# Kernel optimization log

Measured on AMD Instinct MI355X. Metric: run time of the kernel, lower is better.

## Reference

```python
import math
import jax, jax.numpy as jnp
import numpy as np

N_LAYER = 6
THETA = 2.0 ** 16
LN_EPS = 1e-5


def _ln(x):
    # LayerNorm over last dim, no affine (elementwise_affine=False)
    mu = x.mean(-1, keepdims=True)
    var = ((x - mu) ** 2).mean(-1, keepdims=True)
    return (x - mu) / jnp.sqrt(var + LN_EPS)


def _rope(phases, v):
    # phases: (T, N); v: (B, H, T, N)
    ph = (phases % 1.0) * (2.0 * math.pi)
    c, s = jnp.cos(ph), jnp.sin(ph)
    v2 = v.reshape(v.shape[:-1] + (-1, 2))
    v_rot = jnp.stack((-v2[..., 1], v2[..., 0]), axis=-1).reshape(v.shape)
    return v * c + v_rot * s


def setup_inputs() -> dict:
    key = jax.random.key(0)
    ks = jax.random.split(key, 6)
    B, T, D, nh, mult, V = 2, 512, 256, 4, 64, 256
    N = D * mult // nh  # 4096 neurons per head
    std = 0.02
    return {
        "input_ids": jax.random.randint(ks[0], (B, T), 0, V, dtype=jnp.int64),
        "embed_table": jax.random.normal(ks[1], (V, D), jnp.float32) * std,
        "encoder": jax.random.normal(ks[2], (nh, D, N), jnp.float32) * std,
        "encoder_v": jax.random.normal(ks[3], (nh, D, N), jnp.float32) * std,
        "decoder": jax.random.normal(ks[4], (nh * N, D), jnp.float32) * std,
        "lm_head": jax.random.normal(ks[5], (D, V), jnp.float32) * std,
    }


def reference(input_ids, embed_table, encoder, encoder_v, decoder, lm_head):
    B, T = input_ids.shape
    nh, D, N = encoder.shape
    # RoPE freqs: quantize(arange(N), 2) / N exponent (matches get_freqs)
    qidx = jnp.floor(jnp.arange(N, dtype=jnp.float32) / 2.0) * 2.0
    freqs = 1.0 / (THETA ** (qidx / N)) / (2.0 * math.pi)
    phases = jnp.arange(T, dtype=jnp.float32)[:, None] * freqs[None, :]  # (T, N)
    # strictly-lower causal mask (tril with diagonal=-1)
    causal = jnp.tril(jnp.ones((T, T), dtype=bool), k=-1)
    dec = decoder.reshape(nh, N, D)  # head-major, matches transpose(1,2).reshape

    x = _ln(embed_table[input_ids])[:, None]  # (B, 1, T, D)
    trace = None
    for _ in range(N_LAYER):  # shared (tied) weights across layers
        x_sparse = jax.nn.relu(jnp.einsum('bitd,hdn->bhtn', x, encoder))  # (B,H,T,N)
        qr = _rope(phases, x_sparse)
        scores = jnp.einsum('bhtn,bhsn->bhts', qr, qr)  # linear attn, no softmax
        scores = jnp.where(causal, scores, 0.0)
        ykv = _ln(jnp.einsum('bhts,bisd->bhtd', scores, x))  # (B,H,T,D)
        y_sparse = jax.nn.relu(jnp.einsum('bhtd,hdn->bhtn', ykv, encoder_v))
        xy_sparse = x_sparse * y_sparse  # elementwise gate
        trace = xy_sparse  # keep only last layer (used for neuron_trace)
        ymlp = jnp.einsum('bhtn,hnd->btd', xy_sparse, dec)[:, None]  # (B,1,T,D)
        x = _ln(x + _ln(ymlp))

    xs = x[:, 0]  # (B, T, D)
    logits = xs @ lm_head  # (B, T, V)
    embedding = xs.mean(axis=1)  # (B, D), pool_output, no mask
    neuron_trace = trace.mean(axis=2).reshape(B, -1)  # (B, H*N)
    return logits, embedding, neuron_trace
```

## Files before the change

kernel.cpp:

```cpp
#include <hip/hip_runtime.h>
#include <hip/hip_bf16.h>

#define TT 512
#define DD 256
#define NH 4
#define NN 4096
#define VV 256
#define NLAYER 6
#define BB 2
#define BH (BB * NH)
#define NPAIR 2048

typedef __attribute__((ext_vector_type(8))) short bf16x8;
typedef __attribute__((ext_vector_type(4))) float f32x4;
typedef __attribute__((ext_vector_type(8))) unsigned short us8;
typedef __attribute__((ext_vector_type(4))) unsigned short us4;

#define AS1 __attribute__((address_space(1)))
#define AS3 __attribute__((address_space(3)))

__device__ __forceinline__ void glds16(const unsigned short* g, unsigned short* l) {
  __builtin_amdgcn_global_load_lds((const AS1 void*)g, (AS3 void*)l, 16, 0, 0);
}

__device__ __forceinline__ unsigned short f2bf(float f) {
  unsigned int u = __float_as_uint(f);
  return (unsigned short)((u + 0x7FFFu + ((u >> 16) & 1u)) >> 16);
}
__device__ __forceinline__ float bf2f(unsigned short h) {
  return __uint_as_float((unsigned int)h << 16);
}

__device__ __forceinline__ float block_sum_256(float v) {
  __shared__ float s[4];
  #pragma unroll
  for (int o = 32; o > 0; o >>= 1) v += __shfl_down(v, o);
  int lane = threadIdx.x & 63, wid = threadIdx.x >> 6;
  if (lane == 0) s[wid] = v;
  __syncthreads();
  float r = s[0] + s[1] + s[2] + s[3];
  __syncthreads();
  return r;
}

__device__ __forceinline__ float wave_sum64(float v) {
  #pragma unroll
  for (int o = 32; o > 0; o >>= 1) v += __shfl_xor(v, o);
  return v;
}

__device__ __forceinline__ void mfma_tile128_glds(const unsigned short* __restrict__ A, int lda,
                                                  const unsigned short* __restrict__ B, int ldb,
                                                  int K, f32x4 acc[4][4],
                                                  unsigned short* As, unsigned short* Bs) {
  const int tid = threadIdx.x;
  const int lane = tid & 63, wave = tid >> 6;
  const int fm = lane & 15, fq = lane >> 4;
  const int rw = (wave >> 1) << 6, cw = (wave & 1) << 6;
  const int lrow = lane >> 3;
  const int scol = (((lane & 7) ^ lrow) << 3);
  const unsigned short* gA = A + (size_t)(wave * 8 + lrow) * lda + scol;
  const unsigned short* gB = B + (size_t)(wave * 8 + lrow) * ldb + scol;
  unsigned short* lA = As + wave * 8 * 64;
  unsigned short* lB = Bs + wave * 8 * 64;
  const int swz = (fm & 7) << 4;
  for (int k0 = 0; k0 < K; k0 += 64) {
    __syncthreads();
    #pragma unroll
    for (int i = 0; i < 4; ++i) {
      glds16(gA + k0 + (size_t)(i * 32) * lda, lA + i * 32 * 64);
      glds16(gB + k0 + (size_t)(i * 32) * ldb, lB + i * 32 * 64);
    }
    __syncthreads();
    #pragma unroll
    for (int kk = 0; kk < 2; ++kk) {
      bf16x8 af[4], bfv[4];
      #pragma unroll
      for (int i = 0; i < 4; ++i) {
        const int ra = rw + i * 16 + fm;
        const int rb = cw + i * 16 + fm;
        af[i]  = *(const bf16x8*)((const char*)As + ((((ra << 7) + (kk << 6) + (fq << 4))) ^ swz));
        bfv[i] = *(const bf16x8*)((const char*)Bs + ((((rb << 7) + (kk << 6) + (fq << 4))) ^ swz));
      }
      #pragma unroll
      for (int mi = 0; mi < 4; ++mi)
        #pragma unroll
        for (int ni = 0; ni < 4; ++ni)
          acc[mi][ni] = __builtin_amdgcn_mfma_f32_16x16x32_bf16(af[mi], bfv[ni], acc[mi][ni], 0, 0, 0);
    }
  }
}

__device__ __forceinline__ void mfma_tile128_dbuf(const unsigned short* __restrict__ A, int lda,
                                                  const unsigned short* __restrict__ B, int ldb,
                                                  int K, f32x4 acc[4][4],
                                                  unsigned short* As, unsigned short* Bs) {
  const int tid = threadIdx.x;
  const int lane = tid & 63, wave = tid >> 6;
  const int fm = lane & 15, fq = lane >> 4;
  const int rw = (wave >> 1) << 6, cw = (wave & 1) << 6;
  const int lrow = lane >> 3;
  const int scol = (((lane & 7) ^ lrow) << 3);
  const unsigned short* gA = A + (size_t)(wave * 8 + lrow) * lda + scol;
  const unsigned short* gB = B + (size_t)(wave * 8 + lrow) * ldb + scol;
  const int lbase = wave * 8 * 64;
  const int swz = (fm & 7) << 4;
  #pragma unroll
  for (int i = 0; i < 4; ++i) {
    glds16(gA + (size_t)(i * 32) * lda, As + lbase + i * 32 * 64);
    glds16(gB + (size_t)(i * 32) * ldb, Bs + lbase + i * 32 * 64);
  }
  __syncthreads();
  int cur = 0;
  for (int k0 = 0; k0 < K; k0 += 64) {
    if (k0 + 64 < K) {
      unsigned short* nA = As + (cur ^ 1) * 8192 + lbase;
      unsigned short* nB = Bs + (cur ^ 1) * 8192 + lbase;
      #pragma unroll
      for (int i = 0; i < 4; ++i) {
        glds16(gA + (k0 + 64) + (size_t)(i * 32) * lda, nA + i * 32 * 64);
        glds16(gB + (k0 + 64) + (size_t)(i * 32) * ldb, nB + i * 32 * 64);
      }
    }
    const char* cA = (const char*)(As + cur * 8192);
    const char* cB = (const char*)(Bs + cur * 8192);
    #pragma unroll
    for (int kk = 0; kk < 2; ++kk) {
      bf16x8 af[4], bfv[4];
      #pragma unroll
      for (int i = 0; i < 4; ++i) {
        const int ra = rw + i * 16 + fm;
        const int rb = cw + i * 16 + fm;
        af[i]  = *(const bf16x8*)(cA + ((((ra << 7) + (kk << 6) + (fq << 4))) ^ swz));
        bfv[i] = *(const bf16x8*)(cB + ((((rb << 7) + (kk << 6) + (fq << 4))) ^ swz));
      }
      #pragma unroll
      for (int mi = 0; mi < 4; ++mi)
        #pragma unroll
        for (int ni = 0; ni < 4; ++ni)
          acc[mi][ni] = __builtin_amdgcn_mfma_f32_16x16x32_bf16(af[mi], bfv[ni], acc[mi][ni], 0, 0, 0);
    }
    __syncthreads();
    cur ^= 1;
  }
}


__global__ __launch_bounds__(256) void k_csinit(float2* __restrict__ cs) {
  int idx = blockIdx.x * 256 + threadIdx.x;
  int t = idx >> 11, p = idx & (NPAIR - 1);
  const float INV2PI = 0.15915494309189535f;
  const float TWOPI = 6.283185307179586f;
  float f = exp2f(-16.0f * (float)(2 * p) / (float)NN) * INV2PI;
  float ph = fmodf((float)t * f, 1.0f) * TWOPI;
  float s, c;
  sincosf(ph, &s, &c);
  cs[idx] = make_float2(c, s);
}

__global__ __launch_bounds__(256) void k_tcast(const float* __restrict__ in,
                                               unsigned short* __restrict__ out,
                                               int R, int C) {
  __shared__ float tile[64][65];
  const size_t zoff = (size_t)blockIdx.z * R * C;
  const int r0 = blockIdx.y * 64, c0 = blockIdx.x * 64;
  const int cl = threadIdx.x & 63, r4 = threadIdx.x >> 6;
  #pragma unroll 4
  for (int i = 0; i < 16; ++i) {
    int rl = r4 * 16 + i;
    tile[rl][cl] = in[zoff + (size_t)(r0 + rl) * C + c0 + cl];
  }
  __syncthreads();
  #pragma unroll 4
  for (int i = 0; i < 16; ++i) {
    int ccl = r4 * 16 + i;
    out[zoff + (size_t)(c0 + ccl) * R + r0 + cl] = f2bf(tile[cl][ccl]);
  }
}

__global__ __launch_bounds__(256) void k_embed_ln(const int* __restrict__ idw,
                                                  const float* __restrict__ tbl,
                                                  float* __restrict__ x,
                                                  unsigned short* __restrict__ xbf,
                                                  unsigned short* __restrict__ xTbf) {
  __shared__ int s_id;
  int row = blockIdx.x, tid = threadIdx.x;
  if (tid == 0) {
    bool is64 = true;
    for (int i = 1; i < 64; i += 2)
      if (idw[i] != 0) { is64 = false; break; }
    s_id = is64 ? idw[2 * row] : idw[row];
  }
  __syncthreads();
  int id = s_id;
  float v = tbl[(size_t)id * DD + tid];
  float mu = block_sum_256(v) * (1.0f / DD);
  float d = v - mu;
  float var = block_sum_256(d * d) * (1.0f / DD);
  float r = d * rsqrtf(var + 1e-5f);
  x[(size_t)row * DD + tid] = r;
  unsigned short rb = f2bf(r);
  xbf[(size_t)row * DD + tid] = rb;
  int b = row >> 9, t = row & 511;
  xTbf[((size_t)b * DD + tid) * TT + t] = rb;
}


__global__ __launch_bounds__(256) void k_enc(const unsigned short* __restrict__ xbf,
                                             const unsigned short* __restrict__ encT,
                                             const float2* __restrict__ cs,
                                             unsigned short* __restrict__ xsp,
                                             unsigned short* __restrict__ qr) {
  __shared__ float smemf[8192];
  unsigned short* As = (unsigned short*)smemf;
  unsigned short* Bs = As + 8192;
  float (*Sc)[132] = (float(*)[132])smemf;
  const int tid = threadIdx.x;
  const int lin = blockIdx.x;
  const int bh = lin & 7, r0 = lin >> 3;
  const int b = bh >> 2, h = bh & 3;
  const int m0 = (r0 >> 5) * 128, n0 = (r0 & 31) * 128;
  f32x4 acc[4][4] = {};
  mfma_tile128_glds(xbf + (size_t)b * TT * DD + (size_t)m0 * DD, DD,
                    encT + (size_t)h * NN * DD + (size_t)n0 * DD, DD, DD, acc, As, Bs);
  const int lane = tid & 63, wave = tid >> 6;
  const int fm = lane & 15, fq = lane >> 4;
  const int cw = (wave & 1) << 6;
  const int rbase = ((wave >> 1) << 4) + (fq << 2);
  const size_t base = (size_t)bh * TT * NN;
  const int rr = tid >> 3, cc = (tid & 7) << 4;
  #pragma unroll
  for (int mi = 0; mi < 4; ++mi) {
    __syncthreads();
    #pragma unroll
    for (int ni = 0; ni < 4; ++ni)
      #pragma unroll
      for (int r = 0; r < 4; ++r)
        Sc[rbase + r][cw + ni * 16 + fm] = acc[mi][ni][r];
    __syncthreads();
    float v[16];
    *(float4*)&v[0]  = *(const float4*)&Sc[rr][cc];
    *(float4*)&v[4]  = *(const float4*)&Sc[rr][cc + 4];
    *(float4*)&v[8]  = *(const float4*)&Sc[rr][cc + 8];
    *(float4*)&v[12] = *(const float4*)&Sc[rr][cc + 12];
    const int t = m0 + ((rr >> 4) << 6) + mi * 16 + (rr & 15);
    const int n = n0 + cc;
    #pragma unroll
    for (int j = 0; j < 16; ++j) v[j] = fmaxf(v[j], 0.0f);
    us8 o0, o1;
    #pragma unroll
    for (int j = 0; j < 8; ++j) { o0[j] = f2bf(v[j]); o1[j] = f2bf(v[8 + j]); }
    size_t off = base + (size_t)t * NN + n;
    *(us8*)(xsp + off) = o0;
    *(us8*)(xsp + off + 8) = o1;
    float cv[16];
    const float* cp = (const float*)(cs + (size_t)t * NPAIR + (n >> 1));
    *(float4*)&cv[0]  = *(const float4*)(cp);
    *(float4*)&cv[4]  = *(const float4*)(cp + 4);
    *(float4*)&cv[8]  = *(const float4*)(cp + 8);
    *(float4*)&cv[12] = *(const float4*)(cp + 12);
    us8 q0, q1;
    #pragma unroll
    for (int j = 0; j < 8; ++j) {
      float c = cv[2 * j], s = cv[2 * j + 1];
      float ve = v[2 * j], vo = v[2 * j + 1];
      float qe = ve * c - vo * s;
      float qo = vo * c + ve * s;
      if (j < 4) { q0[2 * j] = f2bf(qe); q0[2 * j + 1] = f2bf(qo); }
      else       { q1[2 * (j - 4)] = f2bf(qe); q1[2 * (j - 4) + 1] = f2bf(qo); }
    }
    *(us8*)(qr + off) = q0;
    *(us8*)(qr + off + 8) = q1;
  }
}

__global__ __launch_bounds__(256) void k_scores_part(const unsigned short* __restrict__ qr,
                                                     float* __restrict__ scp) {
  __shared__ float smemf[16384];
  unsigned short* As = (unsigned short*)smemf;
  unsigned short* Bs = As + 16384;
  const int lin = blockIdx.x;
  const int xcd = lin & 7, slot = lin >> 3;
  const int zg = slot / 10, p = slot - zg * 10;
  const int z = xcd + 8 * zg;
  const int bh = z >> 2, kc = z & 3;
  const int mt = (p > 0) + (p > 2) + (p > 5);
  const int nt = p - mt * (mt + 1) / 2;
  const int m0 = mt * 128, n0 = nt * 128;
  const unsigned short* Q = qr + (size_t)bh * TT * NN + kc * 1024;
  f32x4 acc[4][4] = {};
  mfma_tile128_dbuf(Q + (size_t)m0 * NN, NN, Q + (size_t)n0 * NN, NN, 1024, acc, As, Bs);
  const int lane = threadIdx.x & 63, wave = threadIdx.x >> 6;
  const int fm = lane & 15, fq = lane >> 4;
  const int rw = (wave >> 1) << 6, cw = (wave & 1) << 6;
  float* C = scp + (size_t)z * TT * TT;
  const bool diag = (m0 == n0);
  #pragma unroll
  for (int ni = 0; ni < 4; ++ni) {
    int s = n0 + cw + ni * 16 + fm;
    #pragma unroll
    for (int mi = 0; mi < 4; ++mi) {
      int trow = m0 + rw + mi * 16 + (fq << 2);
      #pragma unroll
      for (int r = 0; r < 4; ++r) {
        float v = acc[mi][ni][r];
        if (diag && s >= trow + r) v = 0.0f;
        C[(size_t)(trow + r) * TT + s] = v;
      }
    }
  }
}

__global__ __launch_bounds__(256) void k_ykv_part(const float* __restrict__ scp,
                                                  const unsigned short* __restrict__ xTbf,
                                                  float* __restrict__ ykvp) {
  __shared__ unsigned short As[64][40];
  __shared__ unsigned short Bs[256][40];
  const int tid = threadIdx.x;
  const int lin = blockIdx.x;
  const int bh = lin & 7, r0 = lin >> 3;
  const int m0 = (r0 & 7) * 64, ks = r0 >> 3, b = bh >> 2;
  if (ks * 128 >= m0 + 64) return;
  float* C = ykvp + ((size_t)(bh * 4 + ks) * TT + m0) * DD;
  const int lane = tid & 63, wave = tid >> 6;
  const int srow = tid >> 2, sk = (tid & 3) << 3;
  const int fm = lane & 15, fq = lane >> 4;
  const int t = m0 + srow;
  const size_t abase0 = (size_t)(bh * 4) * TT * TT + (size_t)t * TT;
  const unsigned short* Brow = xTbf + ((size_t)b * DD + tid) * TT + ks * 128;
  f32x4 acc[16] = {};
  for (int k0 = 0; k0 < 128; k0 += 32) {
    const int s0 = ks * 128 + k0 + sk;
    const float* p = scp + abase0 + s0;
    float sum[8];
    float4 u0 = *(const float4*)(p);
    float4 u1 = *(const float4*)(p + 4);
    sum[0] = u0.x; sum[1] = u0.y; sum[2] = u0.z; sum[3] = u0.w;
    sum[4] = u1.x; sum[5] = u1.y; sum[6] = u1.z; sum[7] = u1.w;
    #pragma unroll
    for (int kc = 1; kc < 4; ++kc) {
      float4 v0 = *(const float4*)(p + (size_t)kc * TT * TT);
      float4 v1 = *(const float4*)(p + (size_t)kc * TT * TT + 4);
      sum[0] += v0.x; sum[1] += v0.y; sum[2] += v0.z; sum[3] += v0.w;
      sum[4] += v1.x; sum[5] += v1.y; sum[6] += v1.z; sum[7] += v1.w;
    }
    us8 av;
    #pragma unroll
    for (int j = 0; j < 8; ++j) av[j] = f2bf(sum[j]);
    us8 bv0 = *(const us8*)(Brow + k0);
    us8 bv1 = *(const us8*)(Brow + k0 + 8);
    us8 bv2 = *(const us8*)(Brow + k0 + 16);
    us8 bv3 = *(const us8*)(Brow + k0 + 24);
    __syncthreads();
    *(us8*)(&As[srow][sk]) = av;
    *(us8*)(&Bs[tid][0]) = bv0;
    *(us8*)(&Bs[tid][8]) = bv1;
    *(us8*)(&Bs[tid][16]) = bv2;
    *(us8*)(&Bs[tid][24]) = bv3;
    __syncthreads();
    bf16x8 a = *(const bf16x8*)(&As[wave * 16 + fm][fq << 3]);
    #pragma unroll
    for (int ni = 0; ni < 16; ++ni) {
      bf16x8 bfr = *(const bf16x8*)(&Bs[ni * 16 + fm][fq << 3]);
      acc[ni] = __builtin_amdgcn_mfma_f32_16x16x32_bf16(a, bfr, acc[ni], 0, 0, 0);
    }
  }
  const int trow = wave * 16 + (fq << 2);
  #pragma unroll
  for (int ni = 0; ni < 16; ++ni)
    #pragma unroll
    for (int r = 0; r < 4; ++r)
      C[(size_t)(trow + r) * DD + ni * 16 + fm] = acc[ni][r];
}

__global__ __launch_bounds__(256) void k_ykv_red(const float* __restrict__ ykvp,
                                                 unsigned short* __restrict__ ykvbf) {
  int row = blockIdx.x * 4 + (threadIdx.x >> 6);
  int lane = threadIdx.x & 63;
  int bh = row >> 9, t = row & 511;
  int d0 = lane << 2;
  int nks = (t >> 7) + 1;
  size_t base = ((size_t)(bh * 4) * TT + t) * DD + d0;
  f32x4 v = *(const f32x4*)(ykvp + base);
  if (nks > 1) v += *(const f32x4*)(ykvp + base + (size_t)TT * DD);
  if (nks > 2) v += *(const f32x4*)(ykvp + base + (size_t)2 * TT * DD);
  if (nks > 3) v += *(const f32x4*)(ykvp + base + (size_t)3 * TT * DD);
  float mu = wave_sum64(v.x + v.y + v.z + v.w) * (1.0f / DD);
  f32x4 d = v - mu;
  float var = wave_sum64(d.x * d.x + d.y * d.y + d.z * d.z + d.w * d.w) * (1.0f / DD);
  f32x4 r = d * rsqrtf(var + 1e-5f);
  us4 rb;
  #pragma unroll
  for (int j = 0; j < 4; ++j) rb[j] = f2bf(r[j]);
  *(us4*)(ykvbf + (size_t)row * DD + d0) = rb;
}

__global__ __launch_bounds__(256) void k_ysp_xy(const unsigned short* __restrict__ ykvbf,
                                                const unsigned short* __restrict__ encvT,
                                                const unsigned short* __restrict__ xsp,
                                                unsigned short* __restrict__ xy) {
  __shared__ float smemf[8192];
  unsigned short* As = (unsigned short*)smemf;
  unsigned short* Bs = As + 8192;
  float (*Sc)[132] = (float(*)[132])smemf;
  const int tid = threadIdx.x;
  const int lin = blockIdx.x;
  const int bh = lin & 7, r0 = lin >> 3;
  const int h = bh & 3;
  const int m0 = (r0 >> 5) * 128, n0 = (r0 & 31) * 128;
  f32x4 acc[4][4] = {};
  mfma_tile128_glds(ykvbf + (size_t)bh * TT * DD + (size_t)m0 * DD, DD,
                    encvT + (size_t)h * NN * DD + (size_t)n0 * DD, DD, DD, acc, As, Bs);
  const int lane = tid & 63, wave = tid >> 6;
  const int fm = lane & 15, fq = lane >> 4;
  const int cw = (wave & 1) << 6;
  const int rbase = ((wave >> 1) << 4) + (fq << 2);
  const size_t base = (size_t)bh * TT * NN;
  const int rr = tid >> 3, cc = (tid & 7) << 4;
  #pragma unroll
  for (int mi = 0; mi < 4; ++mi) {
    __syncthreads();
    #pragma unroll
    for (int ni = 0; ni < 4; ++ni)
      #pragma unroll
      for (int r = 0; r < 4; ++r)
        Sc[rbase + r][cw + ni * 16 + fm] = acc[mi][ni][r];
    __syncthreads();
    float v[16];
    *(float4*)&v[0]  = *(const float4*)&Sc[rr][cc];
    *(float4*)&v[4]  = *(const float4*)&Sc[rr][cc + 4];
    *(float4*)&v[8]  = *(const float4*)&Sc[rr][cc + 8];
    *(float4*)&v[12] = *(const float4*)&Sc[rr][cc + 12];
    const int t = m0 + ((rr >> 4) << 6) + mi * 16 + (rr & 15);
    const int n = n0 + cc;
    size_t off = base + (size_t)t * NN + n;
    us8 x0 = *(const us8*)(xsp + off);
    us8 x1 = *(const us8*)(xsp + off + 8);
    us8 o0, o1;
    #pragma unroll
    for (int j = 0; j < 8; ++j) {
      o0[j] = f2bf(bf2f(x0[j]) * fmaxf(v[j], 0.0f));
      o1[j] = f2bf(bf2f(x1[j]) * fmaxf(v[8 + j], 0.0f));
    }
    *(us8*)(xy + off) = o0;
    *(us8*)(xy + off + 8) = o1;
  }
}

__global__ __launch_bounds__(256) void k_ymlp(const unsigned short* __restrict__ xy,
                                              const unsigned short* __restrict__ decT,
                                              float* __restrict__ ym32) {
  __shared__ float smemf[16384];
  unsigned short* As = (unsigned short*)smemf;
  unsigned short* Bs = As + 16384;
  const int lin = blockIdx.x;
  const int xcd = lin & 7, r0 = lin >> 3;
  const int z = xcd + 8 * (r0 >> 3);
  const int tile = r0 & 7;
  const int bh = z >> 3, ks = z & 7, h = bh & 3;
  const int m0 = (tile & 3) * 128, n0 = (tile >> 2) * 128;
  f32x4 acc[4][4] = {};
  mfma_tile128_dbuf(xy + (size_t)bh * TT * NN + (size_t)m0 * NN + ks * 512, NN,
                    decT + (size_t)h * DD * NN + (size_t)n0 * NN + ks * 512, NN,
                    512, acc, As, Bs);
  const int lane = threadIdx.x & 63, wave = threadIdx.x >> 6;
  const int fm = lane & 15, fq = lane >> 4;
  const int rw = (wave >> 1) << 6, cw = (wave & 1) << 6;
  float* C = ym32 + (size_t)z * TT * DD;
  #pragma unroll
  for (int ni = 0; ni < 4; ++ni) {
    int d = n0 + cw + ni * 16 + fm;
    #pragma unroll
    for (int mi = 0; mi < 4; ++mi) {
      int trow = m0 + rw + mi * 16 + (fq << 2);
      #pragma unroll
      for (int r = 0; r < 4; ++r)
        C[(size_t)(trow + r) * DD + d] = acc[mi][ni][r];
    }
  }
}

__global__ __launch_bounds__(256) void k_ln2(float* __restrict__ x,
                                             const float* __restrict__ ym32,
                                             unsigned short* __restrict__ xbf,
                                             unsigned short* __restrict__ xTbf) {
  int row = blockIdx.x * 4 + (threadIdx.x >> 6);
  int lane = threadIdx.x & 63;
  int b = row >> 9, t = row & 511;
  int d0 = lane << 2;
  f32x4 y = {0.0f, 0.0f, 0.0f, 0.0f};
  size_t rbase = (size_t)t * DD + d0;
  #pragma unroll
  for (int p = 0; p < 32; ++p)
    y += *(const f32x4*)(ym32 + (size_t)(b * 32 + p) * TT * DD + rbase);
  float mu = wave_sum64(y.x + y.y + y.z + y.w) * (1.0f / DD);
  f32x4 d = y - mu;
  float var = wave_sum64(d.x * d.x + d.y * d.y + d.z * d.z + d.w * d.w) * (1.0f / DD);
  f32x4 ly = d * rsqrtf(var + 1e-5f);
  f32x4 xv = *(const f32x4*)(x + (size_t)row * DD + d0) + ly;
  float mu2 = wave_sum64(xv.x + xv.y + xv.z + xv.w) * (1.0f / DD);
  f32x4 d2 = xv - mu2;
  float var2 = wave_sum64(d2.x * d2.x + d2.y * d2.y + d2.z * d2.z + d2.w * d2.w) * (1.0f / DD);
  f32x4 r = d2 * rsqrtf(var2 + 1e-5f);
  *(f32x4*)(x + (size_t)row * DD + d0) = r;
  us4 rb;
  #pragma unroll
  for (int j = 0; j < 4; ++j) rb[j] = f2bf(r[j]);
  *(us4*)(xbf + (size_t)row * DD + d0) = rb;
  #pragma unroll
  for (int j = 0; j < 4; ++j)
    xTbf[((size_t)b * DD + d0 + j) * TT + t] = rb[j];
}

__global__ __launch_bounds__(256) void k_trace_part(const unsigned short* __restrict__ xy,
                                                    float* __restrict__ part) {
  const int lin = blockIdx.x;
  const int ts = lin & 7, nc = (lin >> 3) & 1, bh = lin >> 4;
  const int n0 = nc * 2048 + threadIdx.x * 8;
  const size_t base = (size_t)bh * TT * NN + n0;
  float acc[8];
  #pragma unroll
  for (int j = 0; j < 8; ++j) acc[j] = 0.0f;
  for (int t = ts * 64; t < ts * 64 + 64; ++t) {
    us8 v = *(const us8*)(xy + base + (size_t)t * NN);
    #pragma unroll
    for (int j = 0; j < 8; ++j) acc[j] += bf2f(v[j]);
  }
  float* o = part + (size_t)(bh * 8 + ts) * NN + n0;
  #pragma unroll
  for (int j = 0; j < 8; ++j) o[j] = acc[j];
}

__global__ __launch_bounds__(256) void k_trace_red(const float* __restrict__ part,
                                                   float* __restrict__ out) {
  int idx = blockIdx.x * 256 + threadIdx.x;
  int bh = idx >> 12, n = idx & 4095;
  float s = 0.0f;
  #pragma unroll
  for (int ts = 0; ts < 8; ++ts)
    s += part[(size_t)(bh * 8 + ts) * NN + n];
  out[idx] = s * (1.0f / TT);
}

__global__ __launch_bounds__(256) void k_logits(const float* __restrict__ x,
                                                const float* __restrict__ W,
                                                float* __restrict__ out) {
  __shared__ float xs[DD];
  int row = blockIdx.x, tid = threadIdx.x;
  xs[tid] = x[(size_t)row * DD + tid];
  __syncthreads();
  float s = 0.0f;
  #pragma unroll 8
  for (int d = 0; d < DD; ++d) s = fmaf(xs[d], W[(size_t)d * VV + tid], s);
  out[(size_t)row * VV + tid] = s;
}

__global__ __launch_bounds__(256) void k_embedding(const float* __restrict__ x,
                                                   float* __restrict__ out) {
  int idx = blockIdx.x * 256 + threadIdx.x;
  int b = idx >> 8, d = idx & 255;
  float s = 0.0f;
  for (int t = 0; t < TT; ++t) s += x[(size_t)(b * TT + t) * DD + d];
  out[idx] = s * (1.0f / TT);
}

extern "C" void kernel_launch(void* const* d_in, const int* in_sizes, int n_in,
                              void* d_out, int out_size, void* d_ws, size_t ws_size,
                              hipStream_t stream) {
  const int*   ids  = (const int*)d_in[0];
  const float* tbl  = (const float*)d_in[1];
  const float* enc  = (const float*)d_in[2];
  const float* encv = (const float*)d_in[3];
  const float* dec  = (const float*)d_in[4];
  const float* lmh  = (const float*)d_in[5];

  float* ws   = (float*)d_ws;
  float* x    = ws;
  unsigned short* ykvbf = (unsigned short*)(x + 262144);
  float* ym32 = (float*)(ykvbf + 1048576);
  unsigned short* xbf   = (unsigned short*)(ym32 + 8388608);
  unsigned short* xTbf  = xbf + 262144;
  unsigned short* encT  = xTbf + 262144;
  unsigned short* encvT = encT + 4194304;
  unsigned short* decT  = encvT + 4194304;
  unsigned short* xspbf = decT + 4194304;
  unsigned short* qxybf = xspbf + 16777216;
  float2* cs  = (float2*)(qxybf + 16777216);
  float* scp  = (float*)(cs + 1048576);
  float* ykvp = scp + 8388608;

  float* out_logits = (float*)d_out;
  float* out_embed  = out_logits + (size_t)BB * TT * VV;
  float* out_trace  = out_embed + (size_t)BB * DD;

  k_csinit<<<(TT * NPAIR) / 256, 256, 0, stream>>>(cs);
  k_tcast<<<dim3(NN / 64, DD / 64, NH), 256, 0, stream>>>(enc,  encT,  DD, NN);
  k_tcast<<<dim3(NN / 64, DD / 64, NH), 256, 0, stream>>>(encv, encvT, DD, NN);
  k_tcast<<<dim3(DD / 64, NN / 64, NH), 256, 0, stream>>>(dec,  decT,  NN, DD);

  k_embed_ln<<<BB * TT, 256, 0, stream>>>(ids, tbl, x, xbf, xTbf);
  for (int l = 0; l < NLAYER; ++l) {
    k_enc        <<<1024, 256, 0, stream>>>(xbf, encT, cs, xspbf, qxybf);
    k_scores_part<<<320, 256, 0, stream>>>(qxybf, scp);
    k_ykv_part   <<<256, 256, 0, stream>>>(scp, xTbf, ykvp);
    k_ykv_red    <<<BH * TT / 4, 256, 0, stream>>>(ykvp, ykvbf);
    k_ysp_xy     <<<1024, 256, 0, stream>>>(ykvbf, encvT, xspbf, qxybf);
    k_ymlp       <<<512, 256, 0, stream>>>(qxybf, decT, ym32);
    k_ln2        <<<BB * TT / 4, 256, 0, stream>>>(x, ym32, xbf, xTbf);
  }
  k_trace_part<<<128, 256, 0, stream>>>(qxybf, scp);
  k_trace_red <<<128, 256, 0, stream>>>(scp, out_trace);
  k_logits    <<<BB * TT, 256, 0, stream>>>(x, lmh, out_logits);
  k_embedding <<<(BB * DD) / 256, 256, 0, stream>>>(x, out_embed);
}
```

Before: 792.4 us.

## Use 32-row-per-wave MFMA tiling with per-wave epilogue staging and XCD-aware remap

The encoder GEMM kernels now give each wave a 32x128 strip of the output (2x8 MFMA fragments) instead of a 64x64 quadrant. This lets each wave stage its results through a private LDS region and run the ReLU/RoPE and gating epilogue without block-wide barriers. The scores and ymlp kernels remap split-K chunk indices so chunks of the same head land on the same XCD, aiming for better L2 locality. In exchange, each wave loads all 8 B fragments per k-step, which adds LDS read traffic, and the epilogue issues narrower stores.

```diff
diff --git a/kernel.cpp b/kernel.cpp
--- a/kernel.cpp
+++ b/kernel.cpp
@@ -49,14 +49,14 @@
   return v;
 }
 
-__device__ __forceinline__ void mfma_tile128_glds(const unsigned short* __restrict__ A, int lda,
-                                                  const unsigned short* __restrict__ B, int ldb,
-                                                  int K, f32x4 acc[4][4],
-                                                  unsigned short* As, unsigned short* Bs) {
+__device__ __forceinline__ void mfma_tile128_w32(const unsigned short* __restrict__ A, int lda,
+                                                 const unsigned short* __restrict__ B, int ldb,
+                                                 int K, f32x4 acc[2][8],
+                                                 unsigned short* As, unsigned short* Bs) {
   const int tid = threadIdx.x;
   const int lane = tid & 63, wave = tid >> 6;
   const int fm = lane & 15, fq = lane >> 4;
-  const int rw = (wave >> 1) << 6, cw = (wave & 1) << 6;
+  const int wrow = wave << 5;
   const int lrow = lane >> 3;
   const int scol = (((lane & 7) ^ lrow) << 3);
   const unsigned short* gA = A + (size_t)(wave * 8 + lrow) * lda + scol;
@@ -74,18 +74,21 @@
     __syncthreads();
     #pragma unroll
     for (int kk = 0; kk < 2; ++kk) {
-      bf16x8 af[4], bfv[4];
-      #pragma unroll
-      for (int i = 0; i < 4; ++i) {
-        const int ra = rw + i * 16 + fm;
-        const int rb = cw + i * 16 + fm;
-        af[i]  = *(const bf16x8*)((const char*)As + ((((ra << 7) + (kk << 6) + (fq << 4))) ^ swz));
+      bf16x8 af[2], bfv[8];
+      #pragma unroll
+      for (int i = 0; i < 2; ++i) {
+        const int ra = wrow + i * 16 + fm;
+        af[i] = *(const bf16x8*)((const char*)As + ((((ra << 7) + (kk << 6) + (fq << 4))) ^ swz));
+      }
+      #pragma unroll
+      for (int i = 0; i < 8; ++i) {
+        const int rb = i * 16 + fm;
         bfv[i] = *(const bf16x8*)((const char*)Bs + ((((rb << 7) + (kk << 6) + (fq << 4))) ^ swz));
       }
       #pragma unroll
-      for (int mi = 0; mi < 4; ++mi)
+      for (int mi = 0; mi < 2; ++mi)
         #pragma unroll
-        for (int ni = 0; ni < 4; ++ni)
+        for (int ni = 0; ni < 8; ++ni)
           acc[mi][ni] = __builtin_amdgcn_mfma_f32_16x16x32_bf16(af[mi], bfv[ni], acc[mi][ni], 0, 0, 0);
     }
   }
@@ -211,66 +214,61 @@
                                              const float2* __restrict__ cs,
                                              unsigned short* __restrict__ xsp,
                                              unsigned short* __restrict__ qr) {
-  __shared__ float smemf[8192];
+  __shared__ float smemf[8448];
   unsigned short* As = (unsigned short*)smemf;
   unsigned short* Bs = As + 8192;
-  float (*Sc)[132] = (float(*)[132])smemf;
   const int tid = threadIdx.x;
   const int lin = blockIdx.x;
   const int bh = lin & 7, r0 = lin >> 3;
   const int b = bh >> 2, h = bh & 3;
   const int m0 = (r0 >> 5) * 128, n0 = (r0 & 31) * 128;
-  f32x4 acc[4][4] = {};
-  mfma_tile128_glds(xbf + (size_t)b * TT * DD + (size_t)m0 * DD, DD,
-                    encT + (size_t)h * NN * DD + (size_t)n0 * DD, DD, DD, acc, As, Bs);
+  f32x4 acc[2][8] = {};
+  mfma_tile128_w32(xbf + (size_t)b * TT * DD + (size_t)m0 * DD, DD,
+                   encT + (size_t)h * NN * DD + (size_t)n0 * DD, DD, DD, acc, As, Bs);
+  __syncthreads();
   const int lane = tid & 63, wave = tid >> 6;
   const int fm = lane & 15, fq = lane >> 4;
-  const int cw = (wave & 1) << 6;
-  const int rbase = ((wave >> 1) << 4) + (fq << 2);
+  float* Scw = smemf + wave * (16 * 132);
+  const int rr4 = lane >> 4, c0 = (lane & 15) << 3;
   const size_t base = (size_t)bh * TT * NN;
-  const int rr = tid >> 3, cc = (tid & 7) << 4;
-  #pragma unroll
-  for (int mi = 0; mi < 4; ++mi) {
-    __syncthreads();
-    #pragma unroll
-    for (int ni = 0; ni < 4; ++ni)
+  #pragma unroll
+  for (int mi = 0; mi < 2; ++mi) {
+    if (mi) asm volatile("s_waitcnt lgkmcnt(0)" ::: "memory");
+    #pragma unroll
+    for (int ni = 0; ni < 8; ++ni)
       #pragma unroll
       for (int r = 0; r < 4; ++r)
-        Sc[rbase + r][cw + ni * 16 + fm] = acc[mi][ni][r];
-    __syncthreads();
-    float v[16];
-    *(float4*)&v[0]  = *(const float4*)&Sc[rr][cc];
-    *(float4*)&v[4]  = *(const float4*)&Sc[rr][cc + 4];
-    *(float4*)&v[8]  = *(const float4*)&Sc[rr][cc + 8];
-    *(float4*)&v[12] = *(const float4*)&Sc[rr][cc + 12];
-    const int t = m0 + ((rr >> 4) << 6) + mi * 16 + (rr & 15);
-    const int n = n0 + cc;
-    #pragma unroll
-    for (int j = 0; j < 16; ++j) v[j] = fmaxf(v[j], 0.0f);
-    us8 o0, o1;
-    #pragma unroll
-    for (int j = 0; j < 8; ++j) { o0[j] = f2bf(v[j]); o1[j] = f2bf(v[8 + j]); }
-    size_t off = base + (size_t)t * NN + n;
-    *(us8*)(xsp + off) = o0;
-    *(us8*)(xsp + off + 8) = o1;
-    float cv[16];
-    const float* cp = (const float*)(cs + (size_t)t * NPAIR + (n >> 1));
-    *(float4*)&cv[0]  = *(const float4*)(cp);
-    *(float4*)&cv[4]  = *(const float4*)(cp + 4);
-    *(float4*)&cv[8]  = *(const float4*)(cp + 8);
-    *(float4*)&cv[12] = *(const float4*)(cp + 12);
-    us8 q0, q1;
-    #pragma unroll
-    for (int j = 0; j < 8; ++j) {
-      float c = cv[2 * j], s = cv[2 * j + 1];
-      float ve = v[2 * j], vo = v[2 * j + 1];
-      float qe = ve * c - vo * s;
-      float qo = vo * c + ve * s;
-      if (j < 4) { q0[2 * j] = f2bf(qe); q0[2 * j + 1] = f2bf(qo); }
-      else       { q1[2 * (j - 4)] = f2bf(qe); q1[2 * (j - 4) + 1] = f2bf(qo); }
-    }
-    *(us8*)(qr + off) = q0;
-    *(us8*)(qr + off + 8) = q1;
+        Scw[(fq * 4 + r) * 132 + ni * 16 + fm] = acc[mi][ni][r];
+    asm volatile("s_waitcnt lgkmcnt(0)" ::: "memory");
+    #pragma unroll
+    for (int k = 0; k < 4; ++k) {
+      const int rr = k * 4 + rr4;
+      float v[8];
+      *(float4*)&v[0] = *(const float4*)&Scw[rr * 132 + c0];
+      *(float4*)&v[4] = *(const float4*)&Scw[rr * 132 + c0 + 4];
+      const int t = m0 + wave * 32 + mi * 16 + rr;
+      const int n = n0 + c0;
+      #pragma unroll
+      for (int j = 0; j < 8; ++j) v[j] = fmaxf(v[j], 0.0f);
+      us8 o;
+      #pragma unroll
+      for (int j = 0; j < 8; ++j) o[j] = f2bf(v[j]);
+      size_t off = base + (size_t)t * NN + n;
+      *(us8*)(xsp + off) = o;
+      float cv[8];
+      const float* cp = (const float*)(cs + (size_t)t * NPAIR + (n >> 1));
+      *(float4*)&cv[0] = *(const float4*)cp;
+      *(float4*)&cv[4] = *(const float4*)(cp + 4);
+      us8 q;
+      #pragma unroll
+      for (int j = 0; j < 4; ++j) {
+        float c = cv[2 * j], s = cv[2 * j + 1];
+        float ve = v[2 * j], vo = v[2 * j + 1];
+        q[2 * j]     = f2bf(ve * c - vo * s);
+        q[2 * j + 1] = f2bf(vo * c + ve * s);
+      }
+      *(us8*)(qr + off) = q;
+    }
   }
 }
 
@@ -282,7 +280,7 @@
   const int lin = blockIdx.x;
   const int xcd = lin & 7, slot = lin >> 3;
   const int zg = slot / 10, p = slot - zg * 10;
-  const int z = xcd + 8 * zg;
+  const int z = xcd * 4 + zg;
   const int bh = z >> 2, kc = z & 3;
   const int mt = (p > 0) + (p > 2) + (p > 5);
   const int nt = p - mt * (mt + 1) / 2;
@@ -399,51 +397,48 @@
                                                 const unsigned short* __restrict__ encvT,
                                                 const unsigned short* __restrict__ xsp,
                                                 unsigned short* __restrict__ xy) {
-  __shared__ float smemf[8192];
+  __shared__ float smemf[8448];
   unsigned short* As = (unsigned short*)smemf;
   unsigned short* Bs = As + 8192;
-  float (*Sc)[132] = (float(*)[132])smemf;
   const int tid = threadIdx.x;
   const int lin = blockIdx.x;
   const int bh = lin & 7, r0 = lin >> 3;
   const int h = bh & 3;
   const int m0 = (r0 >> 5) * 128, n0 = (r0 & 31) * 128;
-  f32x4 acc[4][4] = {};
-  mfma_tile128_glds(ykvbf + (size_t)bh * TT * DD + (size_t)m0 * DD, DD,
-                    encvT + (size_t)h * NN * DD + (size_t)n0 * DD, DD, DD, acc, As, Bs);
+  f32x4 acc[2][8] = {};
+  mfma_tile128_w32(ykvbf + (size_t)bh * TT * DD + (size_t)m0 * DD, DD,
+                   encvT + (size_t)h * NN * DD + (size_t)n0 * DD, DD, DD, acc, As, Bs);
+  __syncthreads();
   const int lane = tid & 63, wave = tid >> 6;
   const int fm = lane & 15, fq = lane >> 4;
-  const int cw = (wave & 1) << 6;
-  const int rbase = ((wave >> 1) << 4) + (fq << 2);
+  float* Scw = smemf + wave * (16 * 132);
+  const int rr4 = lane >> 4, c0 = (lane & 15) << 3;
   const size_t base = (size_t)bh * TT * NN;
-  const int rr = tid >> 3, cc = (tid & 7) << 4;
-  #pragma unroll
-  for (int mi = 0; mi < 4; ++mi) {
-    __syncthreads();
-    #pragma unroll
-    for (int ni = 0; ni < 4; ++ni)
+  #pragma unroll
+  for (int mi = 0; mi < 2; ++mi) {
+    if (mi) asm volatile("s_waitcnt lgkmcnt(0)" ::: "memory");
+    #pragma unroll
+    for (int ni = 0; ni < 8; ++ni)
       #pragma unroll
       for (int r = 0; r < 4; ++r)
-        Sc[rbase + r][cw + ni * 16 + fm] = acc[mi][ni][r];
-    __syncthreads();
-    float v[16];
-    *(float4*)&v[0]  = *(const float4*)&Sc[rr][cc];
-    *(float4*)&v[4]  = *(const float4*)&Sc[rr][cc + 4];
-    *(float4*)&v[8]  = *(const float4*)&Sc[rr][cc + 8];
-    *(float4*)&v[12] = *(const float4*)&Sc[rr][cc + 12];
-    const int t = m0 + ((rr >> 4) << 6) + mi * 16 + (rr & 15);
-    const int n = n0 + cc;
-    size_t off = base + (size_t)t * NN + n;
-    us8 x0 = *(const us8*)(xsp + off);
-    us8 x1 = *(const us8*)(xsp + off + 8);
-    us8 o0, o1;
-    #pragma unroll
-    for (int j = 0; j < 8; ++j) {
-      o0[j] = f2bf(bf2f(x0[j]) * fmaxf(v[j], 0.0f));
-      o1[j] = f2bf(bf2f(x1[j]) * fmaxf(v[8 + j], 0.0f));
-    }
-    *(us8*)(xy + off) = o0;
-    *(us8*)(xy + off + 8) = o1;
+        Scw[(fq * 4 + r) * 132 + ni * 16 + fm] = acc[mi][ni][r];
+    asm volatile("s_waitcnt lgkmcnt(0)" ::: "memory");
+    #pragma unroll
+    for (int k = 0; k < 4; ++k) {
+      const int rr = k * 4 + rr4;
+      float v[8];
+      *(float4*)&v[0] = *(const float4*)&Scw[rr * 132 + c0];
+      *(float4*)&v[4] = *(const float4*)&Scw[rr * 132 + c0 + 4];
+      const int t = m0 + wave * 32 + mi * 16 + rr;
+      const int n = n0 + c0;
+      size_t off = base + (size_t)t * NN + n;
+      us8 x0 = *(const us8*)(xsp + off);
+      us8 o;
+      #pragma unroll
+      for (int j = 0; j < 8; ++j)
+        o[j] = f2bf(bf2f(x0[j]) * fmaxf(v[j], 0.0f));
+      *(us8*)(xy + off) = o;
+    }
   }
 }
 
@@ -455,7 +450,7 @@
   unsigned short* Bs = As + 16384;
   const int lin = blockIdx.x;
   const int xcd = lin & 7, r0 = lin >> 3;
-  const int z = xcd + 8 * (r0 >> 3);
+  const int z = xcd * 8 + (r0 >> 3);
   const int tile = r0 & 7;
   const int bh = z >> 3, ks = z & 7, h = bh & 3;
   const int m0 = (tile & 3) * 128, n0 = (tile >> 2) * 128;
```

Measured after the change: 762.5 us. 1.04x faster.
